# Optimization experiments

Measured on AMD Instinct MI355X. Metric: run time of the kernel, lower is better.

## Reference

```python
import jax, jax.numpy as jnp
import numpy as np

BLOCK = 8  # block_shape = (8, 8)
INT8_MAX = 127.0  # torch.iinfo(int8).max used by pyblaz bin()


def _dct_matrix(n: int) -> jnp.ndarray:
    """Orthonormal DCT-II matrix D[element, frequency] (pyblaz cosine transform)."""
    e = jnp.arange(n, dtype=jnp.float32)[:, None]
    f = jnp.arange(n, dtype=jnp.float32)[None, :]
    scale = jnp.where(f == 0, jnp.sqrt(1.0 / n), jnp.sqrt(2.0 / n))
    return scale * jnp.cos(jnp.pi * (2.0 * e + 1.0) * f / (2.0 * n))


def setup_inputs() -> dict:
    key = jax.random.key(0)
    x = jax.random.normal(key, (4096, 4096), dtype=jnp.float32)
    return {"x": x}


def reference(x):
    H, W = x.shape
    nb0, nb1 = H // BLOCK, W // BLOCK
    # block splitting: (H, W) -> (nb0, nb1, 8, 8)
    blocked = x.reshape(nb0, BLOCK, nb1, BLOCK).transpose(0, 2, 1, 3)
    D = _dct_matrix(BLOCK)
    # blockwise separable orthogonal transform (same math as the 4D transformer
    # tensor einsum in PyBlaz.blockwise_transform, which is D ⊗ D)
    coeffs = jnp.einsum("abef,eg,fh->abgh", blocked, D, D)
    # mask is all-ones (mask=None) -> masked select == flatten block dims
    flat = coeffs.reshape(nb0, nb1, BLOCK * BLOCK)
    # bin(): per-block max magnitude, then quantize to int8 indices
    biggest = jnp.max(jnp.abs(flat), axis=-1)  # (nb0, nb1)
    safe = jnp.where(biggest == 0, 1.0, biggest)
    indices = jnp.round(flat / safe[..., None] * INT8_MAX).astype(jnp.int8)
    return biggest, indices
```

## Files before the change

### kernel.cpp

```cpp
#include <hip/hip_runtime.h>


#define IMG_W 4096
#define NB    512
#define NBLK  (NB * NB)
#define WG    64

typedef float f32x4 __attribute__((ext_vector_type(4)));

__global__ __launch_bounds__(WG) void dct_quant_kernel(
    const float* __restrict__ x,
    float* __restrict__ out_big,
    float* __restrict__ out_idx)
{
    __shared__ unsigned int lds[WG * 17];

    const int t   = threadIdx.x;
    const int bid = blockIdx.x * WG + t;
    const int bi  = bid >> 9;
    const int bj  = bid & (NB - 1);

    const float s0 = 0.35355339059327373f;
    const float d1 = 0.49039264020161522f;
    const float d2 = 0.46193976625564337f;
    const float d3 = 0.41573480615127262f;
    const float d4 = 0.35355339059327379f;
    const float d5 = 0.27778511650980114f;
    const float d6 = 0.19134171618254492f;
    const float d7 = 0.09754516100806413f;

    const float D[8][8] = {
        { s0,  d1,  d2,  d3,  d4,  d5,  d6,  d7},
        { s0,  d3,  d6, -d7, -d4, -d1, -d2, -d5},
        { s0,  d5, -d6, -d1, -d4,  d7,  d2,  d3},
        { s0,  d7, -d2, -d5,  d4,  d3, -d6, -d1},
        { s0, -d7, -d2,  d5,  d4, -d3, -d6,  d1},
        { s0, -d5, -d6,  d1, -d4, -d7,  d2, -d3},
        { s0, -d3,  d6,  d7, -d4,  d1, -d2,  d5},
        { s0, -d1,  d2, -d3,  d4, -d5,  d6, -d7},
    };

    const float* p = x + (size_t)(bi * 8) * IMG_W + (size_t)bj * 8;

    float C[8][8];
#pragma unroll
    for (int g = 0; g < 8; ++g)
#pragma unroll
        for (int h = 0; h < 8; ++h) C[g][h] = 0.0f;

#pragma unroll
    for (int e = 0; e < 8; ++e) {
        const float4 r0 = *reinterpret_cast<const float4*>(p + (size_t)e * IMG_W);
        const float4 r1 = *reinterpret_cast<const float4*>(p + (size_t)e * IMG_W + 4);
        const float row[8] = {r0.x, r0.y, r0.z, r0.w, r1.x, r1.y, r1.z, r1.w};

        float tmp[8];
#pragma unroll
        for (int h = 0; h < 8; ++h) {
            float acc = row[0] * D[0][h];
#pragma unroll
            for (int f = 1; f < 8; ++f) acc = fmaf(row[f], D[f][h], acc);
            tmp[h] = acc;
        }
#pragma unroll
        for (int g = 0; g < 8; ++g) {
#pragma unroll
            for (int h = 0; h < 8; ++h) C[g][h] = fmaf(D[e][g], tmp[h], C[g][h]);
        }
    }

    float big = 0.0f;
#pragma unroll
    for (int g = 0; g < 8; ++g)
#pragma unroll
        for (int h = 0; h < 8; ++h) big = fmaxf(big, fabsf(C[g][h]));

    __builtin_nontemporal_store(big, &out_big[bid]);

    const float safe = (big == 0.0f) ? 1.0f : big;
    const float inv  = 127.0f / safe;

#pragma unroll
    for (int g = 0; g < 8; ++g) {
        int q[8];
#pragma unroll
        for (int h = 0; h < 8; ++h) q[h] = (int)rintf(C[g][h] * inv);
        const unsigned int w0 = (q[0] & 0xff) | ((q[1] & 0xff) << 8) |
                                ((q[2] & 0xff) << 16) | ((unsigned)(q[3] & 0xff) << 24);
        const unsigned int w1 = (q[4] & 0xff) | ((q[5] & 0xff) << 8) |
                                ((q[6] & 0xff) << 16) | ((unsigned)(q[7] & 0xff) << 24);
        lds[t * 17 + 2 * g]     = w0;
        lds[t * 17 + 2 * g + 1] = w1;
    }

    __syncthreads();

    f32x4* og = reinterpret_cast<f32x4*>(out_idx) + (size_t)blockIdx.x * 1024;
#pragma unroll
    for (int k = 0; k < 16; ++k) {
        const int F = k * WG + t;
        const unsigned int w = lds[(F >> 4) * 17 + (F & 15)];
        f32x4 q;
        q.x = (float)(int)(signed char)(w       & 0xff);
        q.y = (float)(int)(signed char)((w >> 8)  & 0xff);
        q.z = (float)(int)(signed char)((w >> 16) & 0xff);
        q.w = (float)(int)(signed char)(w >> 24);
        __builtin_nontemporal_store(q, &og[F]);
    }
}

extern "C" void kernel_launch(void* const* d_in, const int* in_sizes, int n_in,
                              void* d_out, int out_size, void* d_ws, size_t ws_size,
                              hipStream_t stream) {
    const float* x = (const float*)d_in[0];
    float* out = (float*)d_out;
    float* out_big = out;
    float* out_idx = out + NBLK;

    dct_quant_kernel<<<NBLK / WG, WG, 0, stream>>>(x, out_big, out_idx);
}
```

Measured before the change: 25.73 us.

## Split each 8x8 DCT block across 8 threads with LDS transpose

Instead of one thread computing a whole 8x8 block, each workgroup of 64 threads now handles 8 blocks, with each thread doing one row of the first 1D DCT. Intermediate rows go through an XOR-swizzled LDS tile, the column pass reads the DCT coefficients from a cos-generated LDS table, and the per-block max uses cross-lane shuffles. This is meant to cut per-thread register pressure and give more parallelism and coalesced loads, at the cost of extra LDS traffic, two barriers and 8x more workgroups.

```diff
diff --git a/kernel.cpp b/kernel.cpp
--- a/kernel.cpp
+++ b/kernel.cpp
@@ -13,12 +13,27 @@
     float* __restrict__ out_big,
     float* __restrict__ out_idx)
 {
-    __shared__ unsigned int lds[WG * 17];
+    __shared__ __align__(16) float T[8 * 72];
+    __shared__ float Dl[64];
+    __shared__ unsigned int Sg[8 * 18];
 
-    const int t   = threadIdx.x;
-    const int bid = blockIdx.x * WG + t;
-    const int bi  = bid >> 9;
-    const int bj  = bid & (NB - 1);
+    const int l = threadIdx.x;
+    const int b = l & 7;
+    const int g = l >> 3;
+
+    {
+        float rev = (float)((2 * g + 1) * b) * (1.0f / 32.0f);
+        rev = rev - floorf(rev);
+        float c;
+        asm("v_cos_f32 %0, %1" : "=v"(c) : "v"(rev));
+        const float sc = (b == 0) ? 0.35355339059327373f : 0.5f;
+        Dl[g * 8 + b] = sc * c;
+    }
+
+    const int gblk0 = blockIdx.x * 8;
+    const int gblk  = gblk0 + b;
+    const int bi = gblk >> 9;
+    const int bj = gblk & (NB - 1);
 
     const float s0 = 0.35355339059327373f;
     const float d1 = 0.49039264020161522f;
@@ -28,7 +43,6 @@
     const float d5 = 0.27778511650980114f;
     const float d6 = 0.19134171618254492f;
     const float d7 = 0.09754516100806413f;
-
     const float D[8][8] = {
         { s0,  d1,  d2,  d3,  d4,  d5,  d6,  d7},
         { s0,  d3,  d6, -d7, -d4, -d1, -d2, -d5},
@@ -40,72 +54,77 @@
         { s0, -d1,  d2, -d3,  d4, -d5,  d6, -d7},
     };
 
-    const float* p = x + (size_t)(bi * 8) * IMG_W + (size_t)bj * 8;
+    const float* p = x + (size_t)(bi * 8 + g) * IMG_W + (size_t)bj * 8;
+    const float4 r0 = *reinterpret_cast<const float4*>(p);
+    const float4 r1 = *reinterpret_cast<const float4*>(p + 4);
+    const float row[8] = {r0.x, r0.y, r0.z, r0.w, r1.x, r1.y, r1.z, r1.w};
 
-    float C[8][8];
+    float* tw = &T[b * 72 + g * 8];
 #pragma unroll
-    for (int g = 0; g < 8; ++g)
+    for (int h = 0; h < 8; ++h) {
+        float acc = row[0] * D[0][h];
 #pragma unroll
-        for (int h = 0; h < 8; ++h) C[g][h] = 0.0f;
-
-#pragma unroll
-    for (int e = 0; e < 8; ++e) {
-        const float4 r0 = *reinterpret_cast<const float4*>(p + (size_t)e * IMG_W);
-        const float4 r1 = *reinterpret_cast<const float4*>(p + (size_t)e * IMG_W + 4);
-        const float row[8] = {r0.x, r0.y, r0.z, r0.w, r1.x, r1.y, r1.z, r1.w};
-
-        float tmp[8];
-#pragma unroll
-        for (int h = 0; h < 8; ++h) {
-            float acc = row[0] * D[0][h];
-#pragma unroll
-            for (int f = 1; f < 8; ++f) acc = fmaf(row[f], D[f][h], acc);
-            tmp[h] = acc;
-        }
-#pragma unroll
-        for (int g = 0; g < 8; ++g) {
-#pragma unroll
-            for (int h = 0; h < 8; ++h) C[g][h] = fmaf(D[e][g], tmp[h], C[g][h]);
-        }
-    }
-
-    float big = 0.0f;
-#pragma unroll
-    for (int g = 0; g < 8; ++g)
-#pragma unroll
-        for (int h = 0; h < 8; ++h) big = fmaxf(big, fabsf(C[g][h]));
-
-    __builtin_nontemporal_store(big, &out_big[bid]);
-
-    const float safe = (big == 0.0f) ? 1.0f : big;
-    const float inv  = 127.0f / safe;
-
-#pragma unroll
-    for (int g = 0; g < 8; ++g) {
-        int q[8];
-#pragma unroll
-        for (int h = 0; h < 8; ++h) q[h] = (int)rintf(C[g][h] * inv);
-        const unsigned int w0 = (q[0] & 0xff) | ((q[1] & 0xff) << 8) |
-                                ((q[2] & 0xff) << 16) | ((unsigned)(q[3] & 0xff) << 24);
-        const unsigned int w1 = (q[4] & 0xff) | ((q[5] & 0xff) << 8) |
-                                ((q[6] & 0xff) << 16) | ((unsigned)(q[7] & 0xff) << 24);
-        lds[t * 17 + 2 * g]     = w0;
-        lds[t * 17 + 2 * g + 1] = w1;
+        for (int f = 1; f < 8; ++f) acc = fmaf(row[f], D[f][h], acc);
+        tw[h ^ g] = acc;
     }
 
     __syncthreads();
 
-    f32x4* og = reinterpret_cast<f32x4*>(out_idx) + (size_t)blockIdx.x * 1024;
+    float Dg[8];
 #pragma unroll
-    for (int k = 0; k < 16; ++k) {
-        const int F = k * WG + t;
-        const unsigned int w = lds[(F >> 4) * 17 + (F & 15)];
-        f32x4 q;
-        q.x = (float)(int)(signed char)(w       & 0xff);
-        q.y = (float)(int)(signed char)((w >> 8)  & 0xff);
-        q.z = (float)(int)(signed char)((w >> 16) & 0xff);
-        q.w = (float)(int)(signed char)(w >> 24);
-        __builtin_nontemporal_store(q, &og[F]);
+    for (int e = 0; e < 8; ++e) Dg[e] = Dl[e * 8 + g];
+
+    float C[8];
+#pragma unroll
+    for (int h = 0; h < 8; ++h) C[h] = 0.0f;
+
+    const float* tr = &T[b * 72];
+#pragma unroll
+    for (int e = 0; e < 8; ++e) {
+        const float4 a0 = *reinterpret_cast<const float4*>(tr + e * 8);
+        const float4 a1 = *reinterpret_cast<const float4*>(tr + e * 8 + 4);
+        const float rj[8] = {a0.x, a0.y, a0.z, a0.w, a1.x, a1.y, a1.z, a1.w};
+#pragma unroll
+        for (int h = 0; h < 8; ++h)
+            C[h] = fmaf(Dg[e], rj[h ^ e], C[h]);
+    }
+
+    float m = fabsf(C[0]);
+#pragma unroll
+    for (int h = 1; h < 8; ++h) m = fmaxf(m, fabsf(C[h]));
+    m = fmaxf(m, __shfl_xor(m, 8, 64));
+    m = fmaxf(m, __shfl_xor(m, 16, 64));
+    m = fmaxf(m, __shfl_xor(m, 32, 64));
+
+    if (g == 0)
+        __builtin_nontemporal_store(m, &out_big[gblk0 + b]);
+
+    const float safe = (m == 0.0f) ? 1.0f : m;
+    const float inv  = 127.0f / safe;
+
+    int q[8];
+#pragma unroll
+    for (int h = 0; h < 8; ++h) q[h] = (int)rintf(C[h] * inv);
+    const unsigned int w0 = (q[0] & 0xff) | ((q[1] & 0xff) << 8) |
+                            ((q[2] & 0xff) << 16) | ((unsigned)(q[3] & 0xff) << 24);
+    const unsigned int w1 = (q[4] & 0xff) | ((q[5] & 0xff) << 8) |
+                            ((q[6] & 0xff) << 16) | ((unsigned)(q[7] & 0xff) << 24);
+    Sg[b * 18 + g * 2]     = w0;
+    Sg[b * 18 + g * 2 + 1] = w1;
+
+    __syncthreads();
+
+    f32x4* og = reinterpret_cast<f32x4*>(out_idx + (size_t)gblk0 * 64);
+#pragma unroll
+    for (int kk = 0; kk < 2; ++kk) {
+        const int k = kk * 64 + l;
+        const unsigned int w = Sg[(k >> 4) * 18 + (k & 15)];
+        f32x4 qv;
+        qv.x = (float)(int)(signed char)(w        & 0xff);
+        qv.y = (float)(int)(signed char)((w >> 8)  & 0xff);
+        qv.z = (float)(int)(signed char)((w >> 16) & 0xff);
+        qv.w = (float)(int)(signed char)(w >> 24);
+        __builtin_nontemporal_store(qv, &og[k]);
     }
 }
 
@@ -117,5 +136,5 @@
     float* out_big = out;
     float* out_idx = out + NBLK;
 
-    dct_quant_kernel<<<NBLK / WG, WG, 0, stream>>>(x, out_big, out_idx);
+    dct_quant_kernel<<<NBLK / 8, WG, 0, stream>>>(x, out_big, out_idx);
 }
```

After: 25.29 us. Within noise of the previous version (-1.7%).
